# Kernel tuning notes

Measured on AMD Instinct MI355X. Metric: run time of the kernel, lower is better.

The kernel has to match this reference:

```python
import jax, jax.numpy as jnp
import numpy as np

B, S, H = 2, 2048, 2048
N_HEADS = 16
HEAD_DIM = H // N_HEADS  # 128


def apply_rotary(x, cos, sin):
    # x: (B, n_heads, S, head_dim); cos/sin: (S, head_dim//2)
    d = x.shape[-1] // 2
    x1, x2 = x[..., :d], x[..., d:]
    c = cos[None, None, :x.shape[2]]
    s = sin[None, None, :x.shape[2]]
    return jnp.concatenate([x1 * c - x2 * s, x2 * c + x1 * s], axis=-1)


def setup_inputs() -> dict:
    key = jax.random.key(0)
    k1, k2, k3 = jax.random.split(key, 3)
    x = jax.random.normal(k1, (B, S, H), dtype=jnp.float32)
    qkv_w = jax.random.normal(k2, (3 * H, H), dtype=jnp.float32) * (1.0 / np.sqrt(H))
    o_w = jax.random.normal(k3, (H, H), dtype=jnp.float32) * (1.0 / np.sqrt(H))
    # rotary tables, half head_dim
    inv_freq = 1.0 / (10000.0 ** (jnp.arange(0, HEAD_DIM // 2, dtype=jnp.float32) / (HEAD_DIM // 2)))
    t = jnp.arange(S, dtype=jnp.float32)
    freqs = jnp.outer(t, inv_freq)  # (S, head_dim//2)
    cos, sin = jnp.cos(freqs), jnp.sin(freqs)
    # True = masked (strictly upper triangular)
    causal_mask = jnp.triu(jnp.ones((S, S), dtype=bool), k=1)
    return {"x": x, "qkv_w": qkv_w, "o_w": o_w, "cos": cos, "sin": sin,
            "causal_mask": causal_mask}


def reference(x, qkv_w, o_w, cos, sin, causal_mask):
    Bx, Sx, Hx = x.shape
    qkv = jnp.einsum('bsh,oh->bso', x, qkv_w)  # (B,S,3H)
    qkv = qkv.reshape(Bx, Sx, 3, N_HEADS, HEAD_DIM)
    q, k, v = qkv[:, :, 0], qkv[:, :, 1], qkv[:, :, 2]
    q = jnp.transpose(q, (0, 2, 1, 3))  # (B,nh,S,hd)
    k = jnp.transpose(k, (0, 2, 1, 3))
    v = jnp.transpose(v, (0, 2, 1, 3))
    q = apply_rotary(q, cos, sin)
    k = apply_rotary(k, cos, sin)
    scale = 1.0 / jnp.sqrt(jnp.asarray(HEAD_DIM, dtype=x.dtype))
    attn = jnp.einsum('bnqd,bnkd->bnqk', q, k) * scale
    attn = jnp.where(causal_mask[None, None], -jnp.inf, attn)
    attn = jax.nn.softmax(attn, axis=-1)
    out = jnp.einsum('bnqk,bnkd->bnqd', attn, v)
    out = jnp.transpose(out, (0, 2, 1, 3)).reshape(Bx, Sx, Hx)
    return jnp.einsum('bsh,oh->bso', out, o_w)
```

## Files before the change

kernel.cpp:

```cpp
#include <hip/hip_runtime.h>
#include <hip/hip_bf16.h>
#include <stdint.h>

typedef __attribute__((ext_vector_type(4))) float f32x4;
typedef __attribute__((ext_vector_type(16))) float f32x16;
typedef __attribute__((ext_vector_type(8))) short s16x8;
typedef __attribute__((ext_vector_type(4))) short s16x4;

#define SWZ(g, row) ((((g) & ~7) | (((g) ^ ((row) & 7)) & 7)))
#define SWZ4(g, row) ((g) ^ ((row) & 15))

__device__ __forceinline__ unsigned short f2bf(float f) {
  unsigned u = __builtin_bit_cast(unsigned, f);
  u += 0x7fffu + ((u >> 16) & 1u);
  return (unsigned short)(u >> 16);
}

__device__ __forceinline__ void gld16(const void* g, void* l) {
  __builtin_amdgcn_global_load_lds(
      (const __attribute__((address_space(1))) void*)g,
      (__attribute__((address_space(3))) void*)l, 16, 0, 0);
}

__global__ void cvt_all(const float* __restrict__ x, const float* __restrict__ qkvw,
                        const float* __restrict__ ow, unsigned short* __restrict__ X16,
                        unsigned short* __restrict__ W16, unsigned short* __restrict__ OW16) {
  int i = blockIdx.x * blockDim.x + threadIdx.x;
  const float* src; unsigned short* dst; int off;
  if (i < 2097152)      { src = x;    dst = X16;  off = i; }
  else if (i < 5242880) { src = qkvw; dst = W16;  off = i - 2097152; }
  else                  { src = ow;   dst = OW16; off = i - 5242880; }
  float4 v = ((const float4*)src)[off];
  s16x4 o;
  o[0] = (short)f2bf(v.x); o[1] = (short)f2bf(v.y);
  o[2] = (short)f2bf(v.z); o[3] = (short)f2bf(v.w);
  ((s16x4*)dst)[off] = o;
}

#define PH_PRE \
  __builtin_amdgcn_s_barrier(); \
  asm volatile("s_waitcnt lgkmcnt(0)" ::: "memory"); \
  __builtin_amdgcn_sched_barrier(0); \
  __builtin_amdgcn_s_setprio(1);

#define PH_POST_N \
  __builtin_amdgcn_s_setprio(0); \
  __builtin_amdgcn_s_barrier();

#define PH_POST_W0 \
  __builtin_amdgcn_s_setprio(0); \
  asm volatile("s_waitcnt vmcnt(0)" ::: "memory"); \
  __builtin_amdgcn_s_barrier();

#define PH_POST_W2 \
  __builtin_amdgcn_s_setprio(0); \
  asm volatile("s_waitcnt vmcnt(2)" ::: "memory"); \
  __builtin_amdgcn_s_barrier();

#define PH_POST_W3 \
  __builtin_amdgcn_s_setprio(0); \
  asm volatile("s_waitcnt vmcnt(3)" ::: "memory"); \
  __builtin_amdgcn_s_barrier();

#define RDA(KS) \
  _Pragma("unroll") for (int j = 0; j < 4; ++j) { \
    const int ra = wm * 64 + j * 16 + lg; \
    av[j] = *(const s16x8*)(sA + ra * 128 + (SWZ(4 * (KS) + hg, ra) << 4)); }

#define STG_A(DST, ORG, KT) \
  _Pragma("unroll") for (int rr = 0; rr < 2; ++rr) { \
    const int G = rr * 512 + tid; const int row = G >> 3, g = G & 7; \
    gld16((const char*)((ORG) + (size_t)row * 2048 + (size_t)(KT) * 64) + (SWZ(g, row) << 4), \
          (DST) + rr * 8192 + tid * 16); }

#define STG_B2(DST, ORG, KT, R0) \
  _Pragma("unroll") for (int rr = (R0); rr < (R0) + 2; ++rr) { \
    const int G = rr * 512 + tid; const int row = G >> 3, g = G & 7; \
    gld16((const char*)((ORG) + (size_t)row * 2048 + (size_t)(KT) * 64) + (SWZ(g, row) << 4), \
          (DST) + rr * 8192 + tid * 16); }

#define RDB(KS, CH) \
  _Pragma("unroll") for (int b = 0; b < 3; ++b) { \
    const int bb = (CH) * 3 + b; \
    const int cb = (bb >> 1) * 128 + wn * 16 + (bb & 1) * 64 + lg; \
    bv[b] = *(const s16x8*)(sB + cb * 128 + (SWZ(4 * (KS) + hg, cb) << 4)); }

#define MM12(CH) \
  _Pragma("unroll") for (int j = 0; j < 4; ++j) \
    _Pragma("unroll") for (int b = 0; b < 3; ++b) \
      acc[j][(CH) * 3 + b] = __builtin_amdgcn_mfma_f32_16x16x32_bf16( \
          av[j], bv[b], acc[j][(CH) * 3 + b], 0, 0, 0);

__global__ __launch_bounds__(512, 1) void gemm_qkv_384(
    const unsigned short* __restrict__ A,
    const unsigned short* __restrict__ Bt,
    const float* __restrict__ cosT, const float* __restrict__ sinT,
    unsigned short* __restrict__ qOut, unsigned short* __restrict__ kOut,
    unsigned short* __restrict__ vtOut)
{
  __shared__ char smem[131072];
  const int tid = (int)threadIdx.x;
  const int wid = tid >> 6, l = tid & 63;
  const int lg = l & 15, hg = l >> 4;
  const int wm = wid >> 2, wn = wid & 3;
  const int s = ((int)blockIdx.x & 7) * 64 + ((int)blockIdx.x >> 3);
  const int bm0 = (s & 31) * 128, bn0 = (s >> 5) * 384;

  const unsigned short* Aorg = A + (size_t)bm0 * 2048;
  const unsigned short* Borg = Bt + (size_t)bn0 * 2048;

  f32x4 acc[4][6] = {};

  STG_A(smem + 0, Aorg, 0)
  STG_B2(smem + 16384, Borg, 0, 0)
  STG_B2(smem + 16384, Borg, 0, 2)
  STG_B2(smem + 16384, Borg, 0, 4)
  asm volatile("s_waitcnt vmcnt(3)" ::: "memory");
  __builtin_amdgcn_s_barrier();

  for (int t = 0; t < 31; ++t) {
    const char* sA = smem + (t & 1) * 65536;
    const char* sB = sA + 16384;
    char* dA = smem + ((t & 1) ^ 1) * 65536;
    char* dB = dA + 16384;
    s16x8 av[4], bv[3];
    RDA(0) RDB(0, 0) STG_A(dA, Aorg, t + 1)      PH_PRE MM12(0) PH_POST_W2
    RDB(0, 1)        STG_B2(dB, Borg, t + 1, 0)  PH_PRE MM12(1) PH_POST_N
    RDA(1) RDB(1, 1) STG_B2(dB, Borg, t + 1, 2)  PH_PRE MM12(1) PH_POST_N
    RDB(1, 0)        STG_B2(dB, Borg, t + 1, 4)  PH_PRE MM12(0) PH_POST_W3
  }
  {
    const char* sA = smem + 65536;
    const char* sB = sA + 16384;
    s16x8 av[4], bv[3];
    RDA(0) RDB(0, 0)  PH_PRE MM12(0) PH_POST_W0
    RDB(0, 1)         PH_PRE MM12(1) PH_POST_N
    RDA(1) RDB(1, 1)  PH_PRE MM12(1) PH_POST_N
    RDB(1, 0)         PH_PRE MM12(0)
    __builtin_amdgcn_s_setprio(0);
  }

  #pragma unroll
  for (int j = 0; j < 4; ++j) {
    const int grow0 = bm0 + wm * 64 + j * 16 + hg * 4;
    const int b_ = grow0 >> 11;
    #pragma unroll
    for (int cg = 0; cg < 3; ++cg) {
      const int og = (bn0 >> 7) + cg;
      const int tt = og >> 4, h = og & 15;
      const int d = wn * 16 + lg;
      if (tt < 2) {
        unsigned short* dst = (tt == 0) ? qOut : kOut;
        #pragma unroll
        for (int r = 0; r < 4; ++r) {
          const int gr = grow0 + r;
          const int s1 = gr & 2047;
          const float x1 = acc[j][cg * 2 + 0][r];
          const float x2 = acc[j][cg * 2 + 1][r];
          const float cv = cosT[s1 * 64 + d];
          const float sv = sinT[s1 * 64 + d];
          const size_t base = (((size_t)b_ * 16 + h) * 2048 + s1) * 128;
          dst[base + d]      = f2bf(x1 * cv - x2 * sv);
          dst[base + d + 64] = f2bf(x2 * cv + x1 * sv);
        }
      } else {
        const int s0 = grow0 & 2047;
        s16x4 p1, p2;
        #pragma unroll
        for (int r = 0; r < 4; ++r) {
          p1[r] = (short)f2bf(acc[j][cg * 2 + 0][r]);
          p2[r] = (short)f2bf(acc[j][cg * 2 + 1][r]);
        }
        *(s16x4*)(vtOut + (((size_t)b_ * 16 + h) * 128 + d)      * 2048 + s0) = p1;
        *(s16x4*)(vtOut + (((size_t)b_ * 16 + h) * 128 + d + 64) * 2048 + s0) = p2;
      }
    }
  }
}

#define RDBO(KS, CH) \
  _Pragma("unroll") for (int b = 0; b < 2; ++b) { \
    const int cb = ((CH) * 2 + b) * 64 + wn * 16 + lg; \
    bv[b] = *(const s16x8*)(sB + cb * 128 + (SWZ(4 * (KS) + hg, cb) << 4)); }

#define MMO(CH) \
  _Pragma("unroll") for (int j = 0; j < 4; ++j) \
    _Pragma("unroll") for (int b = 0; b < 2; ++b) \
      acc[j][(CH) * 2 + b] = __builtin_amdgcn_mfma_f32_16x16x32_bf16( \
          av[j], bv[b], acc[j][(CH) * 2 + b], 0, 0, 0);

__global__ __launch_bounds__(512, 1) void gemm_op_256(
    const unsigned short* __restrict__ A,
    const unsigned short* __restrict__ Bt,
    float* __restrict__ C)
{
  __shared__ char smem[98304];
  const int tid = (int)threadIdx.x;
  const int wid = tid >> 6, l = tid & 63;
  const int lg = l & 15, hg = l >> 4;
  const int wm = wid >> 2, wn = wid & 3;
  const int s = ((int)blockIdx.x & 7) * 32 + ((int)blockIdx.x >> 3);
  const int bm0 = (s & 31) * 128, bn0 = (s >> 5) * 256;

  const unsigned short* Aorg = A + (size_t)bm0 * 2048;
  const unsigned short* Borg = Bt + (size_t)bn0 * 2048;

  f32x4 acc[4][4] = {};

  STG_A(smem + 0, Aorg, 0)
  STG_B2(smem + 16384, Borg, 0, 0)
  STG_B2(smem + 16384, Borg, 0, 2)
  asm volatile("s_waitcnt vmcnt(2)" ::: "memory");
  __builtin_amdgcn_s_barrier();

  for (int t = 0; t < 31; ++t) {
    const char* sA = smem + (t & 1) * 49152;
    const char* sB = sA + 16384;
    char* dA = smem + ((t & 1) ^ 1) * 49152;
    char* dB = dA + 16384;
    s16x8 av[4], bv[2];
    RDA(0) RDBO(0, 0) STG_A(dA, Aorg, t + 1)      PH_PRE MMO(0) PH_POST_W2
    RDBO(0, 1)        STG_B2(dB, Borg, t + 1, 0)  PH_PRE MMO(1) PH_POST_N
    RDA(1) RDBO(1, 1) STG_B2(dB, Borg, t + 1, 2)  PH_PRE MMO(1) PH_POST_N
    RDBO(1, 0)                                    PH_PRE MMO(0) PH_POST_W2
  }
  {
    const char* sA = smem + 49152;
    const char* sB = sA + 16384;
    s16x8 av[4], bv[2];
    RDA(0) RDBO(0, 0)  PH_PRE MMO(0) PH_POST_W0
    RDBO(0, 1)         PH_PRE MMO(1) PH_POST_N
    RDA(1) RDBO(1, 1)  PH_PRE MMO(1) PH_POST_N
    RDBO(1, 0)         PH_PRE MMO(0)
    __builtin_amdgcn_s_setprio(0);
  }

  #pragma unroll
  for (int j = 0; j < 4; ++j) {
    const int row0 = bm0 + wm * 64 + j * 16 + hg * 4;
    #pragma unroll
    for (int b = 0; b < 4; ++b) {
      const int col = bn0 + b * 64 + wn * 16 + lg;
      #pragma unroll
      for (int r = 0; r < 4; ++r)
        C[(size_t)(row0 + r) * 2048 + col] = acc[j][b][r];
    }
  }
}

#define ASTG(BB, KV0) \
  _Pragma("unroll") for (int i = 0; i < 4; ++i) { \
    const int G = w * 256 + i * 64 + l; \
    const int rk = G >> 4, gk = G & 15; \
    gld16((const char*)(Kp + qkBase + (size_t)((KV0) + rk) * 128) + (SWZ4(gk, rk) << 4), \
          &sK[BB][w * 4096 + i * 1024]); \
    const int rv = G >> 3, gv = G & 7; \
    gld16((const char*)(Vt + qkBase + (size_t)rv * 2048 + (KV0)) + (SWZ(gv, rv) << 4), \
          &sV[BB][w * 4096 + i * 1024]); \
  }

__global__ __launch_bounds__(256) void attn_fwd(
    const unsigned short* __restrict__ Qp, const unsigned short* __restrict__ Kp,
    const unsigned short* __restrict__ Vt, unsigned short* __restrict__ AO)
{
  __shared__ char sK[2][16384];
  __shared__ char sV[2][16384];
  __shared__ char sP[16384];

  const int tid = (int)threadIdx.x, w = tid >> 6, l = tid & 63;
  const int ql = l & 31, hg2 = l >> 5;
  const int bid = (int)blockIdx.x;
  const int p = bid >> 8, c = bid & 255;
  const int j = c >> 5, bh = c & 31;
  const int qt = p ? (15 - j) : j;
  const size_t qkBase = (size_t)bh * 2048 * 128;
  const int qw0 = qt * 128 + w * 32;
  const int qi = qw0 + ql;
  char* const pw = sP + w * 4096;

  s16x8 qf[8];
  #pragma unroll
  for (int ks = 0; ks < 8; ++ks)
    qf[ks] = *(const s16x8*)(Qp + qkBase + (size_t)(qw0 + ql) * 128 + ks * 16 + hg2 * 8);

  f32x16 ao[4] = {};
  float mrun = -1e30f, lrun = 0.f;
  const float SCALE = 0.08838834764831845f;
  const float L2E = 1.4426950408889634f;
  const float CS = SCALE * L2E;

  const int nkv = 2 * qt + 2;

  ASTG(0, 0)
  ASTG(1, 64)
  asm volatile("s_waitcnt vmcnt(8)" ::: "memory");
  __builtin_amdgcn_s_barrier();

  for (int kv = 0; kv < nkv; ++kv) {
    const int cur = kv & 1;
    const int kv0 = kv * 64;
    const char* cK = sK[cur];
    const char* cV = sV[cur];
    const bool act = (kv0 <= qw0 + 31);

    if (act) {
      f32x16 sS0 = {}, sS1 = {};
      #pragma unroll
      for (int ks = 0; ks < 8; ++ks) {
        s16x8 k0 = *(const s16x8*)(cK + ql * 256 + (SWZ4(2 * ks + hg2, ql) << 4));
        s16x8 k1 = *(const s16x8*)(cK + (32 + ql) * 256 + (SWZ4(2 * ks + hg2, 32 + ql) << 4));
        sS0 = __builtin_amdgcn_mfma_f32_32x32x16_bf16(k0, qf[ks], sS0, 0, 0, 0);
        sS1 = __builtin_amdgcn_mfma_f32_32x32x16_bf16(k1, qf[ks], sS1, 0, 0, 0);
      }

      const bool dg = (kv0 + 63 > qw0);
      if (dg) {
        #pragma unroll
        for (int r = 0; r < 16; ++r) {
          const int jl = (r & 3) + 8 * (r >> 2) + 4 * hg2;
          if (kv0 + jl > qi)      sS0[r] = -1e30f;
          if (kv0 + 32 + jl > qi) sS1[r] = -1e30f;
        }
      }
      float mt = -1e30f;
      #pragma unroll
      for (int r = 0; r < 16; ++r) {
        mt = fmaxf(mt, sS0[r]);
        mt = fmaxf(mt, sS1[r]);
      }
      mt = fmaxf(mt, __shfl_xor(mt, 32));
      mt *= SCALE;
      if (!__all(mt - mrun <= 8.0f)) {
        const float mnew = fmaxf(mrun, mt);
        const float alpha = exp2f((mrun - mnew) * L2E);
        #pragma unroll
        for (int r = 0; r < 16; ++r) {
          const float ar = __shfl(alpha, (r & 3) + 8 * (r >> 2) + 4 * hg2);
          ao[0][r] *= ar; ao[1][r] *= ar; ao[2][r] *= ar; ao[3][r] *= ar;
        }
        lrun *= alpha;
        mrun = mnew;
      }
      const float mL = mrun * L2E;
      float ls = 0.f;
      #pragma unroll
      for (int rq = 0; rq < 4; ++rq) {
        s16x4 pk0, pk1;
        #pragma unroll
        for (int i = 0; i < 4; ++i) {
          const float e0 = exp2f(sS0[rq * 4 + i] * CS - mL); ls += e0; pk0[i] = (short)f2bf(e0);
          const float e1 = exp2f(sS1[rq * 4 + i] * CS - mL); ls += e1; pk1[i] = (short)f2bf(e1);
        }
        *(s16x4*)(pw + ql * 128 + (SWZ(rq, ql) << 4) + hg2 * 8) = pk0;
        *(s16x4*)(pw + ql * 128 + (SWZ(4 + rq, ql) << 4) + hg2 * 8) = pk1;
      }
      ls += __shfl_xor(ls, 32);
      lrun += ls;
      asm volatile("" ::: "memory");

      s16x8 pf[4];
      #pragma unroll
      for (int ks2 = 0; ks2 < 4; ++ks2)
        pf[ks2] = *(const s16x8*)(pw + ql * 128 + (SWZ(2 * ks2 + hg2, ql) << 4));
      #pragma unroll
      for (int db = 0; db < 4; ++db) {
        const int vr = db * 32 + ql;
        #pragma unroll
        for (int ks2 = 0; ks2 < 4; ++ks2) {
          s16x8 vf = *(const s16x8*)(cV + vr * 128 + (SWZ(2 * ks2 + hg2, vr) << 4));
          ao[db] = __builtin_amdgcn_mfma_f32_32x32x16_bf16(pf[ks2], vf, ao[db], 0, 0, 0);
        }
      }
    }

    asm volatile("s_waitcnt lgkmcnt(0)" ::: "memory");
    __builtin_amdgcn_s_barrier();
    if (kv + 2 < nkv) {
      ASTG(cur, kv0 + 128)
      asm volatile("s_waitcnt vmcnt(8)" ::: "memory");
    } else {
      asm volatile("s_waitcnt vmcnt(0)" ::: "memory");
    }
    __builtin_amdgcn_s_barrier();
  }

  float li[16];
  #pragma unroll
  for (int r = 0; r < 16; ++r)
    li[r] = 1.0f / __shfl(lrun, (r & 3) + 8 * (r >> 2) + 4 * hg2);
  const int b = bh >> 4, h = bh & 15;
  #pragma unroll
  for (int db = 0; db < 4; ++db) {
    const int d = h * 128 + db * 32 + ql;
    #pragma unroll
    for (int r = 0; r < 16; ++r) {
      const int q = qw0 + (r & 3) + 8 * (r >> 2) + 4 * hg2;
      AO[((size_t)(b * 2048 + q)) * 2048 + d] = f2bf(ao[db][r] * li[r]);
    }
  }
}

extern "C" void kernel_launch(void* const* d_in, const int* in_sizes, int n_in,
                              void* d_out, int out_size, void* d_ws, size_t ws_size,
                              hipStream_t stream) {
  const float* x    = (const float*)d_in[0];
  const float* qkvw = (const float*)d_in[1];
  const float* ow   = (const float*)d_in[2];
  const float* cosT = (const float*)d_in[3];
  const float* sinT = (const float*)d_in[4];
  float* out = (float*)d_out;

  unsigned short* X16  = (unsigned short*)d_ws;
  unsigned short* W16  = X16  + (size_t)8388608;
  unsigned short* OW16 = W16  + (size_t)12582912;
  unsigned short* Qp   = OW16 + (size_t)4194304;
  unsigned short* Kp   = Qp   + (size_t)8388608;
  unsigned short* Vtp  = Kp   + (size_t)8388608;
  unsigned short* AO   = Vtp  + (size_t)8388608;

  cvt_all<<<24576, 256, 0, stream>>>(x, qkvw, ow, X16, W16, OW16);

  gemm_qkv_384<<<512, 512, 0, stream>>>(X16, W16, cosT, sinT, Qp, Kp, Vtp);

  attn_fwd<<<512, 256, 0, stream>>>(Qp, Kp, Vtp, AO);

  gemm_op_256<<<256, 512, 0, stream>>>(AO, OW16, out);
}
```

Baseline: 240.2 us.

## Replace large-tile QKV and output GEMMs with shared 128x128 two-block-per-CU template

```diff
diff --git a/kernel.cpp b/kernel.cpp
--- a/kernel.cpp
+++ b/kernel.cpp
@@ -52,198 +52,128 @@
   asm volatile("s_waitcnt vmcnt(0)" ::: "memory"); \
   __builtin_amdgcn_s_barrier();
 
-#define PH_POST_W2 \
-  __builtin_amdgcn_s_setprio(0); \
-  asm volatile("s_waitcnt vmcnt(2)" ::: "memory"); \
-  __builtin_amdgcn_s_barrier();
-
-#define PH_POST_W3 \
-  __builtin_amdgcn_s_setprio(0); \
-  asm volatile("s_waitcnt vmcnt(3)" ::: "memory"); \
-  __builtin_amdgcn_s_barrier();
-
-#define RDA(KS) \
+#define STG128(BB, KT) \
+  { char* dA = smem + (BB) * 32768; \
+    char* dB = dA + 16384; \
+    _Pragma("unroll") for (int rr = 0; rr < 4; ++rr) { \
+      const int G = rr * 256 + tid; const int row = G >> 3, g = G & 7; \
+      gld16((const char*)(Aorg + (size_t)row * 2048 + (size_t)(KT) * 64) + (SWZ(g, row) << 4), \
+            dA + rr * 4096 + tid * 16); } \
+    _Pragma("unroll") for (int rr = 0; rr < 4; ++rr) { \
+      const int G = rr * 256 + tid; const int row = G >> 3, g = G & 7; \
+      gld16((const char*)(Borg + (size_t)row * 2048 + (size_t)(KT) * 64) + (SWZ(g, row) << 4), \
+            dB + rr * 4096 + tid * 16); } }
+
+#define RDA4(KS) \
   _Pragma("unroll") for (int j = 0; j < 4; ++j) { \
     const int ra = wm * 64 + j * 16 + lg; \
     av[j] = *(const s16x8*)(sA + ra * 128 + (SWZ(4 * (KS) + hg, ra) << 4)); }
 
-#define STG_A(DST, ORG, KT) \
-  _Pragma("unroll") for (int rr = 0; rr < 2; ++rr) { \
-    const int G = rr * 512 + tid; const int row = G >> 3, g = G & 7; \
-    gld16((const char*)((ORG) + (size_t)row * 2048 + (size_t)(KT) * 64) + (SWZ(g, row) << 4), \
-          (DST) + rr * 8192 + tid * 16); }
-
-#define STG_B2(DST, ORG, KT, R0) \
-  _Pragma("unroll") for (int rr = (R0); rr < (R0) + 2; ++rr) { \
-    const int G = rr * 512 + tid; const int row = G >> 3, g = G & 7; \
-    gld16((const char*)((ORG) + (size_t)row * 2048 + (size_t)(KT) * 64) + (SWZ(g, row) << 4), \
-          (DST) + rr * 8192 + tid * 16); }
-
-#define RDB(KS, CH) \
-  _Pragma("unroll") for (int b = 0; b < 3; ++b) { \
-    const int bb = (CH) * 3 + b; \
-    const int cb = (bb >> 1) * 128 + wn * 16 + (bb & 1) * 64 + lg; \
-    bv[b] = *(const s16x8*)(sB + cb * 128 + (SWZ(4 * (KS) + hg, cb) << 4)); }
-
-#define MM12(CH) \
+#define RDB4(KS) \
+  _Pragma("unroll") for (int f = 0; f < 4; ++f) { \
+    const int cb = wn * 32 + (f & 1) * 16 + (f >> 1) * 64 + lg; \
+    bv[f] = *(const s16x8*)(sB + cb * 128 + (SWZ(4 * (KS) + hg, cb) << 4)); }
+
+#define MM16 \
   _Pragma("unroll") for (int j = 0; j < 4; ++j) \
-    _Pragma("unroll") for (int b = 0; b < 3; ++b) \
-      acc[j][(CH) * 3 + b] = __builtin_amdgcn_mfma_f32_16x16x32_bf16( \
-          av[j], bv[b], acc[j][(CH) * 3 + b], 0, 0, 0);
-
-__global__ __launch_bounds__(512, 1) void gemm_qkv_384(
+    _Pragma("unroll") for (int f = 0; f < 4; ++f) \
+      acc[j][f] = __builtin_amdgcn_mfma_f32_16x16x32_bf16(av[j], bv[f], acc[j][f], 0, 0, 0);
+
+template<int EPI>
+__global__ __launch_bounds__(256, 2) void gemm128(
     const unsigned short* __restrict__ A,
     const unsigned short* __restrict__ Bt,
+    float* __restrict__ C,
     const float* __restrict__ cosT, const float* __restrict__ sinT,
     unsigned short* __restrict__ qOut, unsigned short* __restrict__ kOut,
     unsigned short* __restrict__ vtOut)
 {
-  __shared__ char smem[131072];
+  __shared__ char smem[65536];
   const int tid = (int)threadIdx.x;
   const int wid = tid >> 6, l = tid & 63;
   const int lg = l & 15, hg = l >> 4;
-  const int wm = wid >> 2, wn = wid & 3;
-  const int s = ((int)blockIdx.x & 7) * 64 + ((int)blockIdx.x >> 3);
-  const int bm0 = (s & 31) * 128, bn0 = (s >> 5) * 384;
+  const int wm = wid >> 1, wn = wid & 1;
+  const int cpx = (int)gridDim.x >> 3;
+  const int s = ((int)blockIdx.x & 7) * cpx + ((int)blockIdx.x >> 3);
+  const int bm0 = (s & 31) * 128, bn0 = (s >> 5) * 128;
 
   const unsigned short* Aorg = A + (size_t)bm0 * 2048;
   const unsigned short* Borg = Bt + (size_t)bn0 * 2048;
 
-  f32x4 acc[4][6] = {};
-
-  STG_A(smem + 0, Aorg, 0)
-  STG_B2(smem + 16384, Borg, 0, 0)
-  STG_B2(smem + 16384, Borg, 0, 2)
-  STG_B2(smem + 16384, Borg, 0, 4)
-  asm volatile("s_waitcnt vmcnt(3)" ::: "memory");
+  f32x4 acc[4][4] = {};
+
+  STG128(0, 0)
+  asm volatile("s_waitcnt vmcnt(0)" ::: "memory");
   __builtin_amdgcn_s_barrier();
 
   for (int t = 0; t < 31; ++t) {
-    const char* sA = smem + (t & 1) * 65536;
+    const char* sA = smem + (t & 1) * 32768;
     const char* sB = sA + 16384;
-    char* dA = smem + ((t & 1) ^ 1) * 65536;
-    char* dB = dA + 16384;
-    s16x8 av[4], bv[3];
-    RDA(0) RDB(0, 0) STG_A(dA, Aorg, t + 1)      PH_PRE MM12(0) PH_POST_W2
-    RDB(0, 1)        STG_B2(dB, Borg, t + 1, 0)  PH_PRE MM12(1) PH_POST_N
-    RDA(1) RDB(1, 1) STG_B2(dB, Borg, t + 1, 2)  PH_PRE MM12(1) PH_POST_N
-    RDB(1, 0)        STG_B2(dB, Borg, t + 1, 4)  PH_PRE MM12(0) PH_POST_W3
+    s16x8 av[4], bv[4];
+    RDA4(0) RDB4(0) STG128((t & 1) ^ 1, t + 1)  PH_PRE MM16 PH_POST_N
+    RDA4(1) RDB4(1)                             PH_PRE MM16 PH_POST_W0
   }
   {
-    const char* sA = smem + 65536;
+    const char* sA = smem + 32768;
     const char* sB = sA + 16384;
-    s16x8 av[4], bv[3];
-    RDA(0) RDB(0, 0)  PH_PRE MM12(0) PH_POST_W0
-    RDB(0, 1)         PH_PRE MM12(1) PH_POST_N
-    RDA(1) RDB(1, 1)  PH_PRE MM12(1) PH_POST_N
-    RDB(1, 0)         PH_PRE MM12(0)
+    s16x8 av[4], bv[4];
+    RDA4(0) RDB4(0)  PH_PRE MM16 PH_POST_N
+    RDA4(1) RDB4(1)  PH_PRE MM16
     __builtin_amdgcn_s_setprio(0);
   }
 
-  #pragma unroll
-  for (int j = 0; j < 4; ++j) {
-    const int grow0 = bm0 + wm * 64 + j * 16 + hg * 4;
-    const int b_ = grow0 >> 11;
+  if constexpr (EPI == 0) {
     #pragma unroll
-    for (int cg = 0; cg < 3; ++cg) {
-      const int og = (bn0 >> 7) + cg;
-      const int tt = og >> 4, h = og & 15;
-      const int d = wn * 16 + lg;
+    for (int j = 0; j < 4; ++j) {
+      const int row0 = bm0 + wm * 64 + j * 16 + hg * 4;
+      #pragma unroll
+      for (int f = 0; f < 4; ++f) {
+        const int col = bn0 + wn * 32 + (f & 1) * 16 + (f >> 1) * 64 + lg;
+        #pragma unroll
+        for (int r = 0; r < 4; ++r)
+          C[(size_t)(row0 + r) * 2048 + col] = acc[j][f][r];
+      }
+    }
+  } else {
+    const int og = bn0 >> 7;
+    const int tt = og >> 4, h = og & 15;
+    #pragma unroll
+    for (int j = 0; j < 4; ++j) {
+      const int grow0 = bm0 + wm * 64 + j * 16 + hg * 4;
+      const int b_ = grow0 >> 11;
       if (tt < 2) {
         unsigned short* dst = (tt == 0) ? qOut : kOut;
         #pragma unroll
-        for (int r = 0; r < 4; ++r) {
-          const int gr = grow0 + r;
-          const int s1 = gr & 2047;
-          const float x1 = acc[j][cg * 2 + 0][r];
-          const float x2 = acc[j][cg * 2 + 1][r];
-          const float cv = cosT[s1 * 64 + d];
-          const float sv = sinT[s1 * 64 + d];
-          const size_t base = (((size_t)b_ * 16 + h) * 2048 + s1) * 128;
-          dst[base + d]      = f2bf(x1 * cv - x2 * sv);
-          dst[base + d + 64] = f2bf(x2 * cv + x1 * sv);
+        for (int f = 0; f < 2; ++f) {
+          const int d = wn * 32 + f * 16 + lg;
+          #pragma unroll
+          for (int r = 0; r < 4; ++r) {
+            const int gr = grow0 + r;
+            const int s1 = gr & 2047;
+            const float x1 = acc[j][f][r];
+            const float x2 = acc[j][f + 2][r];
+            const float cv = cosT[s1 * 64 + d];
+            const float sv = sinT[s1 * 64 + d];
+            const size_t base = (((size_t)b_ * 16 + h) * 2048 + s1) * 128;
+            dst[base + d]      = f2bf(x1 * cv - x2 * sv);
+            dst[base + d + 64] = f2bf(x2 * cv + x1 * sv);
+          }
         }
       } else {
         const int s0 = grow0 & 2047;
-        s16x4 p1, p2;
-        #pragma unroll
-        for (int r = 0; r < 4; ++r) {
-          p1[r] = (short)f2bf(acc[j][cg * 2 + 0][r]);
-          p2[r] = (short)f2bf(acc[j][cg * 2 + 1][r]);
-        }
-        *(s16x4*)(vtOut + (((size_t)b_ * 16 + h) * 128 + d)      * 2048 + s0) = p1;
-        *(s16x4*)(vtOut + (((size_t)b_ * 16 + h) * 128 + d + 64) * 2048 + s0) = p2;
-      }
-    }
-  }
-}
-
-#define RDBO(KS, CH) \
-  _Pragma("unroll") for (int b = 0; b < 2; ++b) { \
-    const int cb = ((CH) * 2 + b) * 64 + wn * 16 + lg; \
-    bv[b] = *(const s16x8*)(sB + cb * 128 + (SWZ(4 * (KS) + hg, cb) << 4)); }
-
-#define MMO(CH) \
-  _Pragma("unroll") for (int j = 0; j < 4; ++j) \
-    _Pragma("unroll") for (int b = 0; b < 2; ++b) \
-      acc[j][(CH) * 2 + b] = __builtin_amdgcn_mfma_f32_16x16x32_bf16( \
-          av[j], bv[b], acc[j][(CH) * 2 + b], 0, 0, 0);
-
-__global__ __launch_bounds__(512, 1) void gemm_op_256(
-    const unsigned short* __restrict__ A,
-    const unsigned short* __restrict__ Bt,
-    float* __restrict__ C)
-{
-  __shared__ char smem[98304];
-  const int tid = (int)threadIdx.x;
-  const int wid = tid >> 6, l = tid & 63;
-  const int lg = l & 15, hg = l >> 4;
-  const int wm = wid >> 2, wn = wid & 3;
-  const int s = ((int)blockIdx.x & 7) * 32 + ((int)blockIdx.x >> 3);
-  const int bm0 = (s & 31) * 128, bn0 = (s >> 5) * 256;
-
-  const unsigned short* Aorg = A + (size_t)bm0 * 2048;
-  const unsigned short* Borg = Bt + (size_t)bn0 * 2048;
-
-  f32x4 acc[4][4] = {};
-
-  STG_A(smem + 0, Aorg, 0)
-  STG_B2(smem + 16384, Borg, 0, 0)
-  STG_B2(smem + 16384, Borg, 0, 2)
-  asm volatile("s_waitcnt vmcnt(2)" ::: "memory");
-  __builtin_amdgcn_s_barrier();
-
-  for (int t = 0; t < 31; ++t) {
-    const char* sA = smem + (t & 1) * 49152;
-    const char* sB = sA + 16384;
-    char* dA = smem + ((t & 1) ^ 1) * 49152;
-    char* dB = dA + 16384;
-    s16x8 av[4], bv[2];
-    RDA(0) RDBO(0, 0) STG_A(dA, Aorg, t + 1)      PH_PRE MMO(0) PH_POST_W2
-    RDBO(0, 1)        STG_B2(dB, Borg, t + 1, 0)  PH_PRE MMO(1) PH_POST_N
-    RDA(1) RDBO(1, 1) STG_B2(dB, Borg, t + 1, 2)  PH_PRE MMO(1) PH_POST_N
-    RDBO(1, 0)                                    PH_PRE MMO(0) PH_POST_W2
-  }
-  {
-    const char* sA = smem + 49152;
-    const char* sB = sA + 16384;
-    s16x8 av[4], bv[2];
-    RDA(0) RDBO(0, 0)  PH_PRE MMO(0) PH_POST_W0
-    RDBO(0, 1)         PH_PRE MMO(1) PH_POST_N
-    RDA(1) RDBO(1, 1)  PH_PRE MMO(1) PH_POST_N
-    RDBO(1, 0)         PH_PRE MMO(0)
-    __builtin_amdgcn_s_setprio(0);
-  }
-
-  #pragma unroll
-  for (int j = 0; j < 4; ++j) {
-    const int row0 = bm0 + wm * 64 + j * 16 + hg * 4;
-    #pragma unroll
-    for (int b = 0; b < 4; ++b) {
-      const int col = bn0 + b * 64 + wn * 16 + lg;
-      #pragma unroll
-      for (int r = 0; r < 4; ++r)
-        C[(size_t)(row0 + r) * 2048 + col] = acc[j][b][r];
+        #pragma unroll
+        for (int f = 0; f < 2; ++f) {
+          const int d = wn * 32 + f * 16 + lg;
+          s16x4 p1, p2;
+          #pragma unroll
+          for (int r = 0; r < 4; ++r) {
+            p1[r] = (short)f2bf(acc[j][f][r]);
+            p2[r] = (short)f2bf(acc[j][f + 2][r]);
+          }
+          *(s16x4*)(vtOut + (((size_t)b_ * 16 + h) * 128 + d)      * 2048 + s0) = p1;
+          *(s16x4*)(vtOut + (((size_t)b_ * 16 + h) * 128 + d + 64) * 2048 + s0) = p2;
+        }
+      }
     }
   }
 }
@@ -420,9 +350,10 @@
 
   cvt_all<<<24576, 256, 0, stream>>>(x, qkvw, ow, X16, W16, OW16);
 
-  gemm_qkv_384<<<512, 512, 0, stream>>>(X16, W16, cosT, sinT, Qp, Kp, Vtp);
+  gemm128<1><<<1536, 256, 0, stream>>>(X16, W16, nullptr, cosT, sinT, Qp, Kp, Vtp);
 
   attn_fwd<<<512, 256, 0, stream>>>(Qp, Kp, Vtp, AO);
 
-  gemm_op_256<<<256, 512, 0, stream>>>(AO, OW16, out);
-}
+  gemm128<0><<<512, 256, 0, stream>>>(AO, OW16, out, nullptr, nullptr,
+                                      nullptr, nullptr, nullptr);
+}
```

Result: slower. 253.2 us (+5.4%).
